# Performance work log

Measured on AMD Instinct MI355X. Metric: run time of the kernel, lower is better.

The kernel has to match this reference:

```python
import math
import jax, jax.numpy as jnp
import numpy as np

B, S, E, H, P = 8, 1024, 512, 8, 32
MAXD, OFFS, LW, STL, HID = 256, 8.0, 4, 4, 2048

def _lin(x, w, b):
    return x @ w.T + b

def _gelu(x):
    return jax.nn.gelu(x, approximate=False)  # torch nn.GELU default (erf)

def _ln(x, g, b, eps=1e-5):
    m = x.mean(-1, keepdims=True)
    v = ((x - m) ** 2).mean(-1, keepdims=True)
    return (x - m) / jnp.sqrt(v + eps) * g + b

def setup_inputs() -> dict:
    key = jax.random.key(0)
    ks = iter(jax.random.split(key, 40))
    def w(*shape):
        return (jax.random.normal(next(ks), shape, dtype=jnp.float32) * 0.02)
    x = jax.random.normal(next(ks), (B, S, E), dtype=jnp.float32)
    lengths = jax.random.randint(next(ks), (B,), S // 2, S + 1)
    padding_mask = jnp.arange(S)[None, :] >= lengths[:, None]  # (B,S) bool
    inp = dict(x=x, padding_mask=padding_mask)
    # local MHA (torch nn.MultiheadAttention packed in_proj)
    inp.update(in_proj_w=w(3 * E, E), in_proj_b=jnp.zeros((3 * E,), jnp.float32),
               mha_out_w=w(E, E), mha_out_b=jnp.zeros((E,), jnp.float32))
    # deformable attention projections
    for nm in ('dq', 'dk', 'dv', 'do'):
        inp[nm + '_w'] = w(E, E); inp[nm + '_b'] = jnp.zeros((E,), jnp.float32)
    inp.update(off1_w=w(E, E), off1_b=jnp.zeros((E,), jnp.float32),
               off2_w=w(H * P, E), off2_b=jnp.zeros((H * P,), jnp.float32))
    inp.update(gate1_w=w(E, 3 * E), gate1_b=jnp.zeros((E,), jnp.float32),
               gate2_w=w(E, E), gate2_b=jnp.zeros((E,), jnp.float32))
    inp.update(n1_g=jnp.ones((E,), jnp.float32), n1_b=jnp.zeros((E,), jnp.float32),
               n2_g=jnp.ones((E,), jnp.float32), n2_b=jnp.zeros((E,), jnp.float32))
    inp.update(ffn1_w=w(HID, E), ffn1_b=jnp.zeros((HID,), jnp.float32),
               ffn2_w=w(E, HID), ffn2_b=jnp.zeros((E,), jnp.float32))
    return inp

def _forward(x, padding_mask, in_proj_w, in_proj_b, mha_out_w, mha_out_b,
             dq_w, dq_b, dk_w, dk_b, dv_w, dv_b, do_w, do_b,
             off1_w, off1_b, off2_w, off2_b, gate1_w, gate1_b, gate2_w, gate2_b,
             n1_g, n1_b, n2_g, n2_b, ffn1_w, ffn1_b, ffn2_w, ffn2_b):
    Bv, Sv, Ev = x.shape
    hd = Ev // H
    pos = jnp.arange(Sv)
    # ---------------- local causal windowed MHA ----------------
    qkv = _lin(x, in_proj_w, in_proj_b)
    q, k, v = jnp.split(qkv, 3, axis=-1)
    q = q.reshape(Bv, Sv, H, hd).transpose(0, 2, 1, 3)  # bhsd
    k = k.reshape(Bv, Sv, H, hd).transpose(0, 2, 1, 3)
    v = v.reshape(Bv, Sv, H, hd).transpose(0, 2, 1, 3)
    scores = jnp.einsum('bhqd,bhkd->bhqk', q, k) / math.sqrt(hd)
    future = pos[None, :] > pos[:, None]
    too_far = (pos[:, None] - pos[None, :]) >= min(LW, STL)
    lmask = (future | too_far)[None, None] | padding_mask[:, None, None, :]
    scores = jnp.where(lmask, -jnp.inf, scores)
    allm = lmask.all(-1, keepdims=True)
    scores = jnp.where(allm, 0.0, scores)  # avoid NaN on fully-masked (padded) rows
    attn = jax.nn.softmax(scores, axis=-1)
    attn = jnp.where(lmask, 0.0, attn)
    lo = jnp.einsum('bhqk,bhkd->bhqd', attn, v).transpose(0, 2, 1, 3).reshape(Bv, Sv, Ev)
    local_out = _lin(lo, mha_out_w, mha_out_b)
    # ---------------- deformable long-history attention ----------------
    anchors = jnp.linspace(0.1, 0.9, P)
    valid_len = jnp.clip(Sv - padding_mask.sum(-1), 1, None)
    positions = pos[None, :, None].astype(jnp.float32)  # (1,S,1)
    base = anchors[None, None, :] * positions
    off = jnp.tanh(_lin(_gelu(_lin(x, off1_w, off1_b)), off2_w, off2_b))
    off = off.reshape(Bv, Sv, H, P).mean(2) * OFFS
    sampled = base + off
    sampled = jnp.clip(sampled, jnp.clip(positions - MAXD, 0, None), positions)
    sampled = jnp.minimum(sampled, (valid_len - 1).astype(jnp.float32)[:, None, None])
    sp = jnp.round(sampled).astype(jnp.int32)  # (B,S,P) sample positions
    qd = _lin(x, dq_w, dq_b)
    kd = _lin(x, dk_w, dk_b)
    vd = _lin(x, dv_w, dv_b)
    bidx = jnp.arange(Bv)[:, None, None]
    k_sp = kd[bidx, sp]  # (B,S,P,E) gathered keys
    v_sp = vd[bidx, sp]
    sc = jnp.einsum('bqd,bqpd->bqp', qd, k_sp) / math.sqrt(Ev)
    samp_inv = padding_mask[bidx, sp]
    causal_inv = sp > pos[None, :, None]
    rb = jnp.clip(pos[:, None] - (STL - 1), 0, None)
    long_mem_mask = pos[None, :] >= rb  # (S,S): forbid recent short-term positions
    extra_inv = long_mem_mask[pos[None, :, None], sp]
    inv = samp_inv | causal_inv | extra_inv
    sc = jnp.where(inv, -jnp.inf, sc)
    alli = inv.all(-1, keepdims=True)
    sc = jnp.where(alli, 0.0, sc)
    a = jax.nn.softmax(sc, axis=-1)
    a = jnp.where(inv, 0.0, a)
    long_out = _lin(jnp.einsum('bqp,bqpd->bqd', a, v_sp), do_w, do_b)
    # ---------------- gate fuse + FFN ----------------
    cat = jnp.concatenate([x, local_out, long_out], axis=-1)
    g = jax.nn.sigmoid(_lin(_gelu(_lin(cat, gate1_w, gate1_b)), gate2_w, gate2_b))
    fused = g * local_out + (1.0 - g) * long_out
    x1 = _ln(x + fused, n1_g, n1_b)
    f = _lin(_gelu(_lin(x1, ffn1_w, ffn1_b)), ffn2_w, ffn2_b)
    return _ln(x1 + f, n2_g, n2_b)

def reference(x, padding_mask, in_proj_w, in_proj_b, mha_out_w, mha_out_b,
              dq_w, dq_b, dk_w, dk_b, dv_w, dv_b, do_w, do_b,
              off1_w, off1_b, off2_w, off2_b, gate1_w, gate1_b, gate2_w, gate2_b,
              n1_g, n1_b, n2_g, n2_b, ffn1_w, ffn1_b, ffn2_w, ffn2_b):
    return _forward(x, padding_mask, in_proj_w, in_proj_b, mha_out_w, mha_out_b,
                    dq_w, dq_b, dk_w, dk_b, dv_w, dv_b, do_w, do_b,
                    off1_w, off1_b, off2_w, off2_b, gate1_w, gate1_b, gate2_w, gate2_b,
                    n1_g, n1_b, n2_g, n2_b, ffn1_w, ffn1_b, ffn2_w, ffn2_b)
```

## Files before the change

### kernel.cpp

```cpp
#include <hip/hip_runtime.h>
#include <hip/hip_bf16.h>
#include <type_traits>

typedef __hip_bfloat16 bf16;
typedef __attribute__((ext_vector_type(8))) short short8;
typedef __attribute__((ext_vector_type(4))) float floatx4;

static constexpr int kB = 8;
static constexpr int kS = 1024;
static constexpr int kE = 512;
static constexpr int kH = 8;
static constexpr int kP = 32;
static constexpr int kTok = kB * kS;
static constexpr int kHid = 2048;

__device__ __forceinline__ void load8f(const bf16* p, float* f) {
  uint4 u = *(const uint4*)p;
  const bf16* h = (const bf16*)&u;
#pragma unroll
  for (int e = 0; e < 8; e++) f[e] = __bfloat162float(h[e]);
}
__device__ __forceinline__ void store8b(bf16* p, const float* f) {
  uint4 u;
  bf16* h = (bf16*)&u;
#pragma unroll
  for (int e = 0; e < 8; e++) h[e] = __float2bfloat16(f[e]);
  *(uint4*)p = u;
}
__device__ __forceinline__ bool is_pad(const void* pm, int flag, int idx) {
  return flag ? (((const int*)pm)[idx] != 0)
              : (((const unsigned char*)pm)[idx] != 0);
}
__device__ __forceinline__ float fast_gelu(float x) {
  float u = x * (0.7978845608f + 0.044714998f * x * x);
  float e = __expf(2.0f * u);
  float t = 1.0f - 2.0f / (e + 1.0f);
  return 0.5f * x * (1.0f + t);
}
__device__ __forceinline__ void dma16(const bf16* g, bf16* l) {
  __builtin_amdgcn_global_load_lds(
      (const __attribute__((address_space(1))) unsigned int*)g,
      (__attribute__((address_space(3))) unsigned int*)l, 16, 0, 0);
}
__device__ __forceinline__ void drain_all() { __builtin_amdgcn_s_waitcnt(0); }

__global__ __launch_bounds__(256) void detect_meta_kernel(
    const void* __restrict__ x, const void* __restrict__ pm,
    int* __restrict__ meta) {
  __shared__ int cnt;
  __shared__ int bigfound;
  __shared__ int pc[kB];
  int tid = threadIdx.x;
  if (tid == 0) { cnt = 0; bigfound = 0; }
  if (tid < kB) pc[tid] = 0;
  __syncthreads();
  const unsigned short* u = (const unsigned short*)x;
  int c = 0;
  for (int i = tid; i < 1024; i += 256) {
    int e = (u[i] >> 7) & 0xFF;
    if (e >= 0x90) c++;
  }
  if (c) atomicAdd(&cnt, c);
  const unsigned int* wp = (const unsigned int*)pm;
  int f = 0;
  for (int i = tid; i < 2048; i += 256)
    if (wp[i] & 0xFFFFFFFEu) f = 1;
  if (f) atomicOr(&bigfound, 1);
  __syncthreads();
  int flag = bigfound ? 0 : 1;
  for (int i = tid; i < kTok; i += 256)
    if (is_pad(pm, flag, i)) atomicAdd(&pc[i >> 10], 1);
  __syncthreads();
  if (tid == 0) {
    meta[0] = flag;
    meta[9] = (cnt > 64) ? 1 : 0;
  }
  if (tid < kB) {
    int vl = kS - pc[tid];
    if (vl < 1) vl = 1;
    meta[1 + tid] = vl;
  }
}

struct CvtJob { const void* src; bf16* hi; bf16* lo; int nblk; };
struct CvtJobs { CvtJob j[13]; };
struct CvtFJob { const void* src; float* dst; int n; };
struct CvtFJobs { CvtFJob j[16]; };
__global__ __launch_bounds__(256) void cvt_all_kernel(
    CvtJobs jobs, CvtFJobs fjobs, int totblk, const int* __restrict__ meta) {
  int fp = meta[9];
  int b = blockIdx.x;
  if (b >= totblk) {
#pragma unroll 1
    for (int ji = 0; ji < 16; ji++) {
      CvtFJob J = fjobs.j[ji];
      for (int i = threadIdx.x; i < J.n; i += 256)
        J.dst[i] = fp ? ((const float*)J.src)[i]
                      : __bfloat162float(((const bf16*)J.src)[i]);
    }
    return;
  }
  int ji = 0;
  while (b >= jobs.j[ji].nblk) { b -= jobs.j[ji].nblk; ji++; }
  CvtJob J = jobs.j[ji];
  int i = b * 1024 + threadIdx.x * 4;
  float v[4];
  if (fp) {
    float4 f = ((const float4*)J.src)[i >> 2];
    v[0] = f.x; v[1] = f.y; v[2] = f.z; v[3] = f.w;
  } else {
    uint2 u = *(const uint2*)((const bf16*)J.src + i);
    const bf16* h = (const bf16*)&u;
#pragma unroll
    for (int e = 0; e < 4; e++) v[e] = __bfloat162float(h[e]);
  }
  uint2 uh;
  bf16* hh = (bf16*)&uh;
#pragma unroll
  for (int e = 0; e < 4; e++) hh[e] = __float2bfloat16(v[e]);
  *(uint2*)(J.hi + i) = uh;
  if (J.lo) {
    uint2 ul;
    bf16* hl = (bf16*)&ul;
#pragma unroll
    for (int e = 0; e < 4; e++)
      hl[e] = __float2bfloat16(v[e] - __bfloat162float(hh[e]));
    *(uint2*)(J.lo + i) = ul;
  }
}

static constexpr int BK = 32;

template <int BM, int BN, int ACT, typename OUTT>
__device__ __forceinline__ void gemm_core(bf16* smem, const bf16* A,
                                          const bf16* W, const float* bias,
                                          OUTT* C, int N, int K, int m0,
                                          int n0) {
  constexpr int WR = (BM == 128 && BN == 128) ? 4 : 2;
  constexpr int WC = 4;
  bf16* As[2] = {smem, smem + BM * BK};
  bf16* Bs[2] = {smem + 2 * BM * BK, smem + 2 * BM * BK + BN * BK};
  const int tid = threadIdx.x;
  const int lane = tid & 63;
  const int wid = tid >> 6;
  int wm, wn;
  if constexpr (BM == 128 && BN == 128) {
    wm = (wid >> 1) * 64; wn = (wid & 1) * 64;
  } else {
    wm = wid * 32; wn = 0;
  }

  auto stage = [&](int buf, int kt) {
#pragma unroll
    for (int c = 0; c < BM / 64; c++) {
      int seg = c * 64 + wid * 16;
      int row = seg + (lane >> 2);
      int ch = (lane & 3) ^ ((row >> 1) & 3);
      dma16(&A[(size_t)(m0 + row) * K + kt + ch * 8], &As[buf][seg * BK]);
    }
#pragma unroll
    for (int c = 0; c < BN / 64; c++) {
      int seg = c * 64 + wid * 16;
      int row = seg + (lane >> 2);
      int ch = (lane & 3) ^ ((row >> 1) & 3);
      dma16(&W[(size_t)(n0 + row) * K + kt + ch * 8], &Bs[buf][seg * BK]);
    }
  };

  floatx4 acc[WR][WC];
#pragma unroll
  for (int i = 0; i < WR; i++)
#pragma unroll
    for (int j = 0; j < WC; j++) acc[i][j] = (floatx4)0.0f;

  stage(0, 0);
  drain_all();
  __syncthreads();
  const int niter = K / BK;
  for (int k = 0; k < niter; k++) {
    const int cur = k & 1;
    if (k + 1 < niter) stage(cur ^ 1, (k + 1) * BK);
    const int kb = lane >> 4;
    short8 af[WR], bfr[WC];
#pragma unroll
    for (int i = 0; i < WR; i++) {
      int r = wm + i * 16 + (lane & 15);
      af[i] = *(const short8*)(&As[cur][r * BK + ((kb ^ ((r >> 1) & 3)) << 3)]);
    }
#pragma unroll
    for (int j = 0; j < WC; j++) {
      int r = wn + j * 16 + (lane & 15);
      bfr[j] = *(const short8*)(&Bs[cur][r * BK + ((kb ^ ((r >> 1) & 3)) << 3)]);
    }
#pragma unroll
    for (int i = 0; i < WR; i++)
#pragma unroll
      for (int j = 0; j < WC; j++)
        acc[i][j] = __builtin_amdgcn_mfma_f32_16x16x32_bf16(bfr[j], af[i],
                                                            acc[i][j], 0, 0, 0);
    drain_all();
    __syncthreads();
  }

#pragma unroll
  for (int i = 0; i < WR; i++) {
    int row = m0 + wm + i * 16 + (lane & 15);
#pragma unroll
    for (int j = 0; j < WC; j++) {
      int col = n0 + wn + j * 16 + ((lane >> 4) << 2);
      float bv[4] = {0.f, 0.f, 0.f, 0.f};
      if (bias) {
        float4 b4 = *(const float4*)&bias[col];
        bv[0] = b4.x; bv[1] = b4.y; bv[2] = b4.z; bv[3] = b4.w;
      }
      float v[4];
#pragma unroll
      for (int r = 0; r < 4; r++) {
        v[r] = acc[i][j][r] + bv[r];
        if (ACT == 1) v[r] = fast_gelu(v[r]);
        else if (ACT == 2) v[r] = 1.0f / (1.0f + __expf(-v[r]));
      }
      size_t idx = (size_t)row * N + col;
      if constexpr (std::is_same<OUTT, float>::value) {
        *(float4*)&C[idx] = make_float4(v[0], v[1], v[2], v[3]);
      } else {
        uint2 u;
        bf16* h = (bf16*)&u;
#pragma unroll
        for (int r = 0; r < 4; r++) h[r] = __float2bfloat16(v[r]);
        *(uint2*)&C[idx] = u;
      }
    }
  }
}

template <int BM, int BN, bool SPLIT, bool ALWAYS_AL>
__device__ __forceinline__ void gemm3_core(
    bf16* smem, const bf16* Ah, const bf16* Al, const bf16* Wh,
    const bf16* Wl, const float* bias, const int* meta, float* Cf, bf16* Chi,
    bf16* Clo, int N, int K, int m0, int n0) {
  constexpr int WR = 2;
  constexpr int WC = (BM == 128) ? 4 : 2;
  bf16* Ash = smem;
  bf16* Asl = smem + BM * BK;
  bf16* Bsh = smem + 2 * BM * BK;
  bf16* Bsl = smem + 2 * BM * BK + BN * BK;
  const int fp = meta[9];
  const bool use_al = fp || ALWAYS_AL;
  const int tid = threadIdx.x;
  const int lane = tid & 63;
  const int wid = tid >> 6;
  int wm, wn;
  if constexpr (BM == 128) {
    wm = wid * 32; wn = 0;
  } else {
    wm = (wid >> 1) * 32; wn = (wid & 1) * 32;
  }

  floatx4 acc[WR][WC];
#pragma unroll
  for (int i = 0; i < WR; i++)
#pragma unroll
    for (int j = 0; j < WC; j++) acc[i][j] = (floatx4)0.0f;

  for (int kt = 0; kt < K; kt += BK) {
#pragma unroll
    for (int c = 0; c < BM / 64; c++) {
      int seg = c * 64 + wid * 16;
      int row = seg + (lane >> 2);
      int ch = (lane & 3) ^ ((row >> 1) & 3);
      size_t g = (size_t)(m0 + row) * K + kt + ch * 8;
      dma16(&Ah[g], &Ash[seg * BK]);
      if (use_al) dma16(&Al[g], &Asl[seg * BK]);
    }
#pragma unroll
    for (int c = 0; c < BN / 64; c++) {
      int seg = c * 64 + wid * 16;
      int row = seg + (lane >> 2);
      int ch = (lane & 3) ^ ((row >> 1) & 3);
      size_t g = (size_t)(n0 + row) * K + kt + ch * 8;
      dma16(&Wh[g], &Bsh[seg * BK]);
      if (fp) dma16(&Wl[g], &Bsl[seg * BK]);
    }
    drain_all();
    __syncthreads();
    const int kb = lane >> 4;
    short8 ah[WR], al[WR], bh[WC], bl[WC];
#pragma unroll
    for (int i = 0; i < WR; i++) {
      int r = wm + i * 16 + (lane & 15);
      int ro = r * BK + ((kb ^ ((r >> 1) & 3)) << 3);
      ah[i] = *(const short8*)(&Ash[ro]);
      if (use_al) al[i] = *(const short8*)(&Asl[ro]);
    }
#pragma unroll
    for (int j = 0; j < WC; j++) {
      int r = wn + j * 16 + (lane & 15);
      int ro = r * BK + ((kb ^ ((r >> 1) & 3)) << 3);
      bh[j] = *(const short8*)(&Bsh[ro]);
      if (fp) bl[j] = *(const short8*)(&Bsl[ro]);
    }
#pragma unroll
    for (int i = 0; i < WR; i++)
#pragma unroll
      for (int j = 0; j < WC; j++) {
        acc[i][j] = __builtin_amdgcn_mfma_f32_16x16x32_bf16(bh[j], ah[i],
                                                            acc[i][j], 0, 0, 0);
        if (fp)
          acc[i][j] = __builtin_amdgcn_mfma_f32_16x16x32_bf16(
              bl[j], ah[i], acc[i][j], 0, 0, 0);
        if (use_al)
          acc[i][j] = __builtin_amdgcn_mfma_f32_16x16x32_bf16(
              bh[j], al[i], acc[i][j], 0, 0, 0);
      }
    __syncthreads();
  }

#pragma unroll
  for (int i = 0; i < WR; i++) {
    int row = m0 + wm + i * 16 + (lane & 15);
#pragma unroll
    for (int j = 0; j < WC; j++) {
      int col = n0 + wn + j * 16 + ((lane >> 4) << 2);
      float4 b4 = *(const float4*)&bias[col];
      float bv[4] = {b4.x, b4.y, b4.z, b4.w};
      if constexpr (SPLIT) {
        uint2 uh, ul;
        bf16* hh = (bf16*)&uh;
        bf16* hl = (bf16*)&ul;
#pragma unroll
        for (int r = 0; r < 4; r++) {
          float v = acc[i][j][r] + bv[r];
          float g = 0.5f * v * (1.0f + erff(v * 0.70710678118654752f));
          bf16 hi = __float2bfloat16(g);
          hh[r] = hi;
          hl[r] = __float2bfloat16(g - __bfloat162float(hi));
        }
        *(uint2*)&Chi[(size_t)row * N + col] = uh;
        *(uint2*)&Clo[(size_t)row * N + col] = ul;
      } else {
        *(float4*)&Cf[(size_t)row * N + col] =
            make_float4(acc[i][j][0] + bv[0], acc[i][j][1] + bv[1],
                        acc[i][j][2] + bv[2], acc[i][j][3] + bv[3]);
      }
    }
  }
}

template <int BM, int BN, int ACT, typename OUTT>
__global__ __launch_bounds__(256) void gemm_bt(
    const bf16* __restrict__ A, const bf16* __restrict__ W,
    const float* __restrict__ bias, OUTT* __restrict__ C, int N, int K) {
  __shared__ bf16 smem[2 * (BM + BN) * BK];
  gemm_core<BM, BN, ACT, OUTT>(smem, A, W, bias, C, N, K, blockIdx.x * BM,
                               blockIdx.y * BN);
}

__global__ __launch_bounds__(256) void gemm_pair(
    const bf16* __restrict__ A0, const bf16* __restrict__ W0,
    const float* __restrict__ b0, bf16* __restrict__ C0,
    const bf16* __restrict__ A1, const bf16* __restrict__ W1,
    const float* __restrict__ b1, bf16* __restrict__ C1, int N, int K) {
  __shared__ bf16 smem[2 * (128 + 64) * BK];
  int nb = N >> 6;
  bool s = (int)blockIdx.y >= nb;
  gemm_core<128, 64, 0, bf16>(smem, s ? A1 : A0, s ? W1 : W0, s ? b1 : b0,
                              s ? C1 : C0, N, K, blockIdx.x * 128,
                              (s ? (int)blockIdx.y - nb : (int)blockIdx.y) * 64);
}

__global__ __launch_bounds__(256) void qkv_o1_kernel(
    const bf16* __restrict__ x_hi, const bf16* __restrict__ x_lo,
    const bf16* __restrict__ wall, const float* __restrict__ ball,
    bf16* __restrict__ qkv_all, const bf16* __restrict__ o1h,
    const bf16* __restrict__ o1l, const float* __restrict__ o1b,
    const int* __restrict__ meta, bf16* __restrict__ h_hi,
    bf16* __restrict__ h_lo) {
  __shared__ bf16 smem[2 * 256 * BK];
  if ((int)blockIdx.y < 24) {
    gemm_core<128, 128, 0, bf16>(smem, x_hi, wall, ball, qkv_all, 3072, kE,
                                 blockIdx.x * 128, blockIdx.y * 128);
  } else {
    gemm3_core<128, 64, true, false>(smem, x_hi, x_lo, o1h, o1l, o1b, meta,
                                     nullptr, h_hi, h_lo, kE, kE,
                                     blockIdx.x * 128,
                                     ((int)blockIdx.y - 24) * 64);
  }
}

__device__ __forceinline__ void local_attn_body(const bf16* __restrict__ qkv,
                                                const void* __restrict__ pm,
                                                const int* __restrict__ meta,
                                                bf16* __restrict__ lo,
                                                int bid) {
  int lane = threadIdx.x & 63;
  int t = bid * 4 + (threadIdx.x >> 6);
  int b = t >> 10, s = t & 1023;
  int h = lane >> 3, sub = lane & 7;
  int flag = meta[0];
  float q[8];
  load8f(qkv + (size_t)t * 3072 + h * 64 + sub * 8, q);
  float sc[4];
  bool val[4];
#pragma unroll
  for (int w = 0; w < 4; w++) {
    int kp = s - 3 + w;
    bool v = (kp >= 0) && !is_pad(pm, flag, b * kS + kp);
    float d = 0.0f;
    if (v) {
      float kk[8];
      load8f(qkv + (size_t)(b * kS + kp) * 3072 + 512 + h * 64 + sub * 8, kk);
#pragma unroll
      for (int e = 0; e < 8; e++) d += q[e] * kk[e];
    }
    d += __shfl_xor(d, 1);
    d += __shfl_xor(d, 2);
    d += __shfl_xor(d, 4);
    sc[w] = v ? d / 8.0f : -INFINITY;
    val[w] = v;
  }
  float mx = fmaxf(fmaxf(sc[0], sc[1]), fmaxf(sc[2], sc[3]));
  float a[4] = {0.f, 0.f, 0.f, 0.f};
  if (mx != -INFINITY) {
    float ssum = 0.f;
#pragma unroll
    for (int w = 0; w < 4; w++) {
      float e = val[w] ? expf(sc[w] - mx) : 0.0f;
      a[w] = e;
      ssum += e;
    }
#pragma unroll
    for (int w = 0; w < 4; w++) a[w] /= ssum;
  }
  float o[8] = {0.f, 0.f, 0.f, 0.f, 0.f, 0.f, 0.f, 0.f};
#pragma unroll
  for (int w = 0; w < 4; w++) {
    if (val[w] && a[w] > 0.0f) {
      int kp = s - 3 + w;
      float vv[8];
      load8f(qkv + (size_t)(b * kS + kp) * 3072 + 1024 + h * 64 + sub * 8, vv);
#pragma unroll
      for (int e = 0; e < 8; e++) o[e] += a[w] * vv[e];
    }
  }
  store8b(lo + (size_t)t * kE + lane * 8, o);
}

__global__ __launch_bounds__(256) void local_o2_kernel(
    const bf16* __restrict__ qkv, const void* __restrict__ pm,
    const int* __restrict__ meta, bf16* __restrict__ lo_ctx,
    const bf16* __restrict__ h_hi, const bf16* __restrict__ h_lo,
    const bf16* __restrict__ o2h, const bf16* __restrict__ o2l,
    const float* __restrict__ o2b, float* __restrict__ rawf) {
  __shared__ bf16 smem[4 * 64 * BK];
  if ((int)blockIdx.x < 2048) {
    local_attn_body(qkv, pm, meta, lo_ctx, blockIdx.x);
  } else {
    int id = (int)blockIdx.x - 2048;
    gemm3_core<64, 64, false, true>(smem, h_hi, h_lo, o2h, o2l, o2b, meta,
                                    rawf, nullptr, nullptr, 256, kE,
                                    (id >> 2) * 64, (id & 3) * 64);
  }
}

__global__ __launch_bounds__(256) void long_attn_kernel(
    const bf16* __restrict__ qkv, const float* __restrict__ rawf,
    const void* __restrict__ pm, const int* __restrict__ meta,
    bf16* __restrict__ ctx) {
  int lane = threadIdx.x & 63;
  int bid = blockIdx.x;
  int sbid = (bid & 7) * 256 + (bid >> 3);
  int t = sbid * 4 + (threadIdx.x >> 6);
  int b = t >> 10, s = t & 1023;
  int flag = meta[0];
  int p = lane & 31;
  float off = 0.0f;
#pragma unroll
  for (int h = 0; h < kH; h++) off += tanhf(rawf[(size_t)t * 256 + h * kP + p]);
  double anchor = 0.1 + 0.8 * (double)p / 31.0;
  double sampled = anchor * (double)s + (double)off;
  double lov = fmax(0.0, (double)s - 256.0);
  sampled = fmin(fmax(sampled, lov), (double)s);
  int vlen = meta[1 + b];
  sampled = fmin(sampled, (double)(vlen - 1));
  int spv = (int)rint(sampled);
  bool inv = is_pad(pm, flag, b * kS + spv) || (spv > s) ||
             (spv >= max(0, s - 3));
  int row_abs = b * kS + spv;
  float q[8];
  load8f(qkv + (size_t)t * 3072 + 1536 + lane * 8, q);
  float sc_mine = 0.0f;
#pragma unroll 4
  for (int pp = 0; pp < 32; pp++) {
    int row = __shfl(row_abs, pp);
    float kk[8];
    load8f(qkv + (size_t)row * 3072 + 2048 + lane * 8, kk);
    float d = 0.0f;
#pragma unroll
    for (int e = 0; e < 8; e++) d += q[e] * kk[e];
#pragma unroll
    for (int m = 1; m < 64; m <<= 1) d += __shfl_xor(d, m);
    if (p == pp) sc_mine = d;
  }
  float sc = inv ? -INFINITY : sc_mine / 22.627416997969522f;
  float mx = sc;
#pragma unroll
  for (int m = 1; m < 32; m <<= 1) mx = fmaxf(mx, __shfl_xor(mx, m));
  float e = (inv || mx == -INFINITY) ? 0.0f : expf(sc - mx);
  float ssum = e;
#pragma unroll
  for (int m = 1; m < 32; m <<= 1) ssum += __shfl_xor(ssum, m);
  float a = (ssum > 0.0f) ? e / ssum : 0.0f;
  float o[8] = {0.f, 0.f, 0.f, 0.f, 0.f, 0.f, 0.f, 0.f};
#pragma unroll 4
  for (int pp = 0; pp < 32; pp++) {
    float ap = __shfl(a, pp);
    int row = __shfl(row_abs, pp);
    if (ap != 0.0f) {
      float vv[8];
      load8f(qkv + (size_t)row * 3072 + 2560 + lane * 8, vv);
#pragma unroll
      for (int e2 = 0; e2 < 8; e2++) o[e2] += ap * vv[e2];
    }
  }
  store8b(ctx + (size_t)t * kE + lane * 8, o);
}

__global__ __launch_bounds__(256) void gemm_gate1(
    const bf16* __restrict__ x, const bf16* __restrict__ lo,
    const bf16* __restrict__ lg, const bf16* __restrict__ W,
    const float* __restrict__ bias, bf16* __restrict__ C) {
  constexpr int BM = 128, BN = 64, WR = 2, WC = 4;
  constexpr int N = 512, K = 1536;
  __shared__ bf16 As[2][BM * BK];
  __shared__ bf16 Bs[2][BN * BK];
  const int tid = threadIdx.x;
  const int lane = tid & 63;
  const int wid = tid >> 6;
  const int wm = wid * 32, wn = 0;
  const int m0 = blockIdx.x * BM, n0 = blockIdx.y * BN;

  auto stage = [&](int buf, int kt) {
    const bf16* src = (kt < 512) ? x : (kt < 1024) ? lo : lg;
    int kk = kt & 511;
#pragma unroll
    for (int c = 0; c < 2; c++) {
      int seg = c * 64 + wid * 16;
      int row = seg + (lane >> 2);
      int ch = (lane & 3) ^ ((row >> 1) & 3);
      dma16(&src[(size_t)(m0 + row) * 512 + kk + ch * 8], &As[buf][seg * BK]);
    }
    {
      int seg = wid * 16;
      int row = seg + (lane >> 2);
      int ch = (lane & 3) ^ ((row >> 1) & 3);
      dma16(&W[(size_t)(n0 + row) * K + kt + ch * 8], &Bs[buf][seg * BK]);
    }
  };

  floatx4 acc[WR][WC];
#pragma unroll
  for (int i = 0; i < WR; i++)
#pragma unroll
    for (int j = 0; j < WC; j++) acc[i][j] = (floatx4)0.0f;

  stage(0, 0);
  drain_all();
  __syncthreads();
  const int niter = K / BK;
  for (int k = 0; k < niter; k++) {
    const int cur = k & 1;
    if (k + 1 < niter) stage(cur ^ 1, (k + 1) * BK);
    const int kb = lane >> 4;
    short8 af[WR], bfr[WC];
#pragma unroll
    for (int i = 0; i < WR; i++) {
      int r = wm + i * 16 + (lane & 15);
      af[i] = *(const short8*)(&As[cur][r * BK + ((kb ^ ((r >> 1) & 3)) << 3)]);
    }
#pragma unroll
    for (int j = 0; j < WC; j++) {
      int r = wn + j * 16 + (lane & 15);
      bfr[j] = *(const short8*)(&Bs[cur][r * BK + ((kb ^ ((r >> 1) & 3)) << 3)]);
    }
#pragma unroll
    for (int i = 0; i < WR; i++)
#pragma unroll
      for (int j = 0; j < WC; j++)
        acc[i][j] = __builtin_amdgcn_mfma_f32_16x16x32_bf16(bfr[j], af[i],
                                                            acc[i][j], 0, 0, 0);
    drain_all();
    __syncthreads();
  }

#pragma unroll
  for (int i = 0; i < WR; i++) {
    int row = m0 + wm + i * 16 + (lane & 15);
#pragma unroll
    for (int j = 0; j < WC; j++) {
      int col = n0 + wn + j * 16 + ((lane >> 4) << 2);
      float4 b4 = *(const float4*)&bias[col];
      float bv[4] = {b4.x, b4.y, b4.z, b4.w};
      uint2 u;
      bf16* h = (bf16*)&u;
#pragma unroll
      for (int r = 0; r < 4; r++)
        h[r] = __float2bfloat16(fast_gelu(acc[i][j][r] + bv[r]));
      *(uint2*)&C[(size_t)row * N + col] = u;
    }
  }
}

__global__ __launch_bounds__(256) void ln1_kernel(
    const void* __restrict__ xin, const int* __restrict__ meta,
    const bf16* __restrict__ lo, const bf16* __restrict__ lg,
    const bf16* __restrict__ g, const float* __restrict__ gamma,
    const float* __restrict__ beta, bf16* __restrict__ x1b,
    float* __restrict__ x1f) {
  int lane = threadIdx.x & 63;
  int t = blockIdx.x * 4 + (threadIdx.x >> 6);
  size_t base = (size_t)t * kE + lane * 8;
  float xv[8], lov[8], lgv[8], gv[8], h[8];
  if (meta[9]) {
    const float4* xf = (const float4*)((const float*)xin + base);
    float4 a = xf[0], b2 = xf[1];
    xv[0] = a.x; xv[1] = a.y; xv[2] = a.z; xv[3] = a.w;
    xv[4] = b2.x; xv[5] = b2.y; xv[6] = b2.z; xv[7] = b2.w;
  } else {
    load8f((const bf16*)xin + base, xv);
  }
  load8f(lo + base, lov);
  load8f(lg + base, lgv);
  load8f(g + base, gv);
  float s1 = 0.f, s2 = 0.f;
#pragma unroll
  for (int e = 0; e < 8; e++) {
    h[e] = xv[e] + gv[e] * lov[e] + (1.0f - gv[e]) * lgv[e];
    s1 += h[e];
    s2 += h[e] * h[e];
  }
#pragma unroll
  for (int m = 1; m < 64; m <<= 1) {
    s1 += __shfl_xor(s1, m);
    s2 += __shfl_xor(s2, m);
  }
  float mean = s1 * (1.0f / kE);
  float var = s2 * (1.0f / kE) - mean * mean;
  float rstd = 1.0f / sqrtf(var + 1e-5f);
  float y[8];
#pragma unroll
  for (int e = 0; e < 8; e++)
    y[e] = (h[e] - mean) * rstd * gamma[lane * 8 + e] + beta[lane * 8 + e];
  store8b(x1b + base, y);
#pragma unroll
  for (int e = 0; e < 8; e++) x1f[base + e] = y[e];
}

__global__ __launch_bounds__(256) void ln2_kernel(
    const float* __restrict__ x1f, const float* __restrict__ ff,
    const float* __restrict__ gamma, const float* __restrict__ beta,
    const int* __restrict__ meta, void* __restrict__ out) {
  int lane = threadIdx.x & 63;
  int t = blockIdx.x * 4 + (threadIdx.x >> 6);
  size_t base = (size_t)t * kE + lane * 8;
  float h[8];
  float s1 = 0.f, s2 = 0.f;
#pragma unroll
  for (int e = 0; e < 8; e++) {
    h[e] = x1f[base + e] + ff[base + e];
    s1 += h[e];
    s2 += h[e] * h[e];
  }
#pragma unroll
  for (int m = 1; m < 64; m <<= 1) {
    s1 += __shfl_xor(s1, m);
    s2 += __shfl_xor(s2, m);
  }
  float mean = s1 * (1.0f / kE);
  float var = s2 * (1.0f / kE) - mean * mean;
  float rstd = 1.0f / sqrtf(var + 1e-5f);
  float y[8];
#pragma unroll
  for (int e = 0; e < 8; e++)
    y[e] = (h[e] - mean) * rstd * gamma[lane * 8 + e] + beta[lane * 8 + e];
  if (meta[9]) {
    float* of = (float*)out + base;
    ((float4*)of)[0] = make_float4(y[0], y[1], y[2], y[3]);
    ((float4*)of)[1] = make_float4(y[4], y[5], y[6], y[7]);
  } else {
    store8b((bf16*)out + base, y);
  }
}

extern "C" void kernel_launch(void* const* d_in, const int* in_sizes, int n_in,
                              void* d_out, int out_size, void* d_ws,
                              size_t ws_size, hipStream_t stream) {
  const void* x = d_in[0];
  const void* pm = d_in[1];

  char* w = (char*)d_ws;
  auto alloc = [&](size_t bytes) {
    char* p = w;
    w += (bytes + 255) & ~(size_t)255;
    return p;
  };
  bf16* qkv_all = (bf16*)alloc((size_t)kTok * 3072 * 2);
  bf16* lo_ctx = (bf16*)alloc((size_t)kTok * kE * 2);
  bf16* ctx2 = (bf16*)alloc((size_t)kTok * kE * 2);
  bf16* local_out = (bf16*)alloc((size_t)kTok * kE * 2);
  bf16* long_out = (bf16*)alloc((size_t)kTok * kE * 2);
  bf16* hbuf = (bf16*)alloc((size_t)kTok * kE * 2);
  bf16* gbuf = (bf16*)alloc((size_t)kTok * kE * 2);
  bf16* x1b = (bf16*)alloc((size_t)kTok * kE * 2);
  float* x1f = (float*)alloc((size_t)kTok * kE * 4);
  float* rawf = (float*)alloc((size_t)kTok * 256 * 4);
  int* meta = (int*)alloc(256);
  bf16* x_hi = (bf16*)alloc((size_t)kTok * kE * 2);
  bf16* x_lo = (bf16*)alloc((size_t)kTok * kE * 2);
  bf16* wall = (bf16*)alloc((size_t)3072 * 512 * 2);
  bf16* mow = (bf16*)alloc(512 * 512 * 2);
  bf16* dow = (bf16*)alloc(512 * 512 * 2);
  bf16* o1h = (bf16*)alloc(512 * 512 * 2);
  bf16* o1l = (bf16*)alloc(512 * 512 * 2);
  bf16* o2h = (bf16*)alloc(256 * 512 * 2);
  bf16* o2l = (bf16*)alloc(256 * 512 * 2);
  bf16* g1w = (bf16*)alloc(512 * 1536 * 2);
  bf16* g2w = (bf16*)alloc(512 * 512 * 2);
  bf16* f1w = (bf16*)alloc((size_t)2048 * 512 * 2);
  bf16* f2w = (bf16*)alloc((size_t)512 * 2048 * 2);
  float* ball = (float*)alloc(3072 * 4);
  float* mob = (float*)alloc(512 * 4);
  float* dob = (float*)alloc(512 * 4);
  float* o1b = (float*)alloc(512 * 4);
  float* o2b = (float*)alloc(256 * 4);
  float* g1b = (float*)alloc(512 * 4);
  float* g2b = (float*)alloc(512 * 4);
  float* n1g = (float*)alloc(512 * 4);
  float* n1bt = (float*)alloc(512 * 4);
  float* n2g = (float*)alloc(512 * 4);
  float* n2bt = (float*)alloc(512 * 4);
  float* f1b = (float*)alloc(2048 * 4);
  float* f2b = (float*)alloc(512 * 4);

  bf16* h_hi = hbuf;
  bf16* h_lo = x1b;
  float* f_f32 = (float*)qkv_all;
  bf16* ffn_h = (bf16*)((char*)qkv_all + (size_t)kTok * kE * 4);

  dim3 blk(256);
  detect_meta_kernel<<<1, blk, 0, stream>>>(x, pm, meta);

  CvtJobs J;
  auto job = [](const void* s, bf16* hi, bf16* lo, int n) {
    CvtJob j; j.src = s; j.hi = hi; j.lo = lo; j.nblk = n >> 10; return j;
  };
  J.j[0] = job(d_in[0], x_hi, x_lo, kTok * kE);
  J.j[1] = job(d_in[2], wall, nullptr, 1536 * 512);
  J.j[2] = job(d_in[6], wall + (size_t)1536 * 512, nullptr, 512 * 512);
  J.j[3] = job(d_in[8], wall + (size_t)2048 * 512, nullptr, 512 * 512);
  J.j[4] = job(d_in[10], wall + (size_t)2560 * 512, nullptr, 512 * 512);
  J.j[5] = job(d_in[4], mow, nullptr, 512 * 512);
  J.j[6] = job(d_in[12], dow, nullptr, 512 * 512);
  J.j[7] = job(d_in[14], o1h, o1l, 512 * 512);
  J.j[8] = job(d_in[16], o2h, o2l, 256 * 512);
  J.j[9] = job(d_in[18], g1w, nullptr, 512 * 1536);
  J.j[10] = job(d_in[20], g2w, nullptr, 512 * 512);
  J.j[11] = job(d_in[26], f1w, nullptr, 2048 * 512);
  J.j[12] = job(d_in[28], f2w, nullptr, 512 * 2048);
  int totblk = 0;
  for (int i = 0; i < 13; i++) totblk += J.j[i].nblk;

  CvtFJobs JF;
  auto fjob = [](const void* s, float* d, int n) {
    CvtFJob j; j.src = s; j.dst = d; j.n = n; return j;
  };
  JF.j[0] = fjob(d_in[3], ball, 1536);
  JF.j[1] = fjob(d_in[7], ball + 1536, 512);
  JF.j[2] = fjob(d_in[9], ball + 2048, 512);
  JF.j[3] = fjob(d_in[11], ball + 2560, 512);
  JF.j[4] = fjob(d_in[5], mob, 512);
  JF.j[5] = fjob(d_in[13], dob, 512);
  JF.j[6] = fjob(d_in[15], o1b, 512);
  JF.j[7] = fjob(d_in[17], o2b, 256);
  JF.j[8] = fjob(d_in[19], g1b, 512);
  JF.j[9] = fjob(d_in[21], g2b, 512);
  JF.j[10] = fjob(d_in[22], n1g, 512);
  JF.j[11] = fjob(d_in[23], n1bt, 512);
  JF.j[12] = fjob(d_in[24], n2g, 512);
  JF.j[13] = fjob(d_in[25], n2bt, 512);
  JF.j[14] = fjob(d_in[27], f1b, 2048);
  JF.j[15] = fjob(d_in[29], f2b, 512);
  cvt_all_kernel<<<totblk + 1, blk, 0, stream>>>(J, JF, totblk, meta);

  qkv_o1_kernel<<<dim3(64, 32), blk, 0, stream>>>(
      x_hi, x_lo, wall, ball, qkv_all, o1h, o1l, o1b, meta, h_hi, h_lo);
  local_o2_kernel<<<2560, blk, 0, stream>>>(qkv_all, pm, meta, lo_ctx, h_hi,
                                            h_lo, o2h, o2l, o2b, rawf);
  long_attn_kernel<<<2048, blk, 0, stream>>>(qkv_all, rawf, pm, meta, ctx2);

  gemm_pair<<<dim3(64, 16), blk, 0, stream>>>(lo_ctx, mow, mob, local_out,
                                              ctx2, dow, dob, long_out, kE, kE);

  gemm_gate1<<<dim3(64, 8), blk, 0, stream>>>(x_hi, local_out, long_out, g1w,
                                              g1b, hbuf);
  gemm_bt<128, 64, 2, bf16><<<dim3(64, 8), blk, 0, stream>>>(
      hbuf, g2w, g2b, gbuf, kE, kE);

  ln1_kernel<<<2048, blk, 0, stream>>>(x, meta, local_out, long_out, gbuf, n1g,
                                       n1bt, x1b, x1f);
  gemm_bt<128, 128, 1, bf16><<<dim3(64, 16), blk, 0, stream>>>(
      x1b, f1w, f1b, ffn_h, kHid, kE);
  gemm_bt<128, 64, 0, float><<<dim3(64, 8), blk, 0, stream>>>(
      ffn_h, f2w, f2b, f_f32, kE, kHid);
  ln2_kernel<<<2048, blk, 0, stream>>>(x1f, f_f32, n2g, n2bt, meta, d_out);
}
```

Before: 503.5 us.

## Read bf16 inputs directly in GEMMs and skip conversion pass when not fp32

When inputs are already bf16, the conversion kernel now exits early and each GEMM selects the raw input and weight pointers at runtime instead of reading converted copies. The QKV GEMM maps column tiles onto separate raw weight tensors. It also splits the previously fused qkv+o1 and local_attn+o2 launches into separate kernels. This removes a full copy pass over weights and activations in the bf16 case, at the cost of more kernel launches and the loss of the overlap the fused launches gave.

```diff
diff --git a/kernel.cpp b/kernel.cpp
--- a/kernel.cpp
+++ b/kernel.cpp
@@ -100,20 +100,13 @@
     }
     return;
   }
+  if (!fp) return;
   int ji = 0;
   while (b >= jobs.j[ji].nblk) { b -= jobs.j[ji].nblk; ji++; }
   CvtJob J = jobs.j[ji];
   int i = b * 1024 + threadIdx.x * 4;
-  float v[4];
-  if (fp) {
-    float4 f = ((const float4*)J.src)[i >> 2];
-    v[0] = f.x; v[1] = f.y; v[2] = f.z; v[3] = f.w;
-  } else {
-    uint2 u = *(const uint2*)((const bf16*)J.src + i);
-    const bf16* h = (const bf16*)&u;
-#pragma unroll
-    for (int e = 0; e < 4; e++) v[e] = __bfloat162float(h[e]);
-  }
+  float4 f = ((const float4*)J.src)[i >> 2];
+  float v[4] = {f.x, f.y, f.z, f.w};
   uint2 uh;
   bf16* hh = (bf16*)&uh;
 #pragma unroll
@@ -135,7 +128,7 @@
 __device__ __forceinline__ void gemm_core(bf16* smem, const bf16* A,
                                           const bf16* W, const float* bias,
                                           OUTT* C, int N, int K, int m0,
-                                          int n0) {
+                                          int n0, int n0w) {
   constexpr int WR = (BM == 128 && BN == 128) ? 4 : 2;
   constexpr int WC = 4;
   bf16* As[2] = {smem, smem + BM * BK};
@@ -163,7 +156,7 @@
       int seg = c * 64 + wid * 16;
       int row = seg + (lane >> 2);
       int ch = (lane & 3) ^ ((row >> 1) & 3);
-      dma16(&W[(size_t)(n0 + row) * K + kt + ch * 8], &Bs[buf][seg * BK]);
+      dma16(&W[(size_t)(n0w + row) * K + kt + ch * 8], &Bs[buf][seg * BK]);
     }
   };
 
@@ -237,7 +230,7 @@
 template <int BM, int BN, bool SPLIT, bool ALWAYS_AL>
 __device__ __forceinline__ void gemm3_core(
     bf16* smem, const bf16* Ah, const bf16* Al, const bf16* Wh,
-    const bf16* Wl, const float* bias, const int* meta, float* Cf, bf16* Chi,
+    const bf16* Wl, const float* bias, int fp, float* Cf, bf16* Chi,
     bf16* Clo, int N, int K, int m0, int n0) {
   constexpr int WR = 2;
   constexpr int WC = (BM == 128) ? 4 : 2;
@@ -245,7 +238,6 @@
   bf16* Asl = smem + BM * BK;
   bf16* Bsh = smem + 2 * BM * BK;
   bf16* Bsl = smem + 2 * BM * BK + BN * BK;
-  const int fp = meta[9];
   const bool use_al = fp || ALWAYS_AL;
   const int tid = threadIdx.x;
   const int lane = tid & 63;
@@ -347,54 +339,182 @@
   }
 }
 
+__global__ __launch_bounds__(256) void gemm_qkv(
+    const bf16* __restrict__ xc, const void* __restrict__ xr,
+    const bf16* __restrict__ wall, const void* __restrict__ ipr,
+    const void* __restrict__ dqr, const void* __restrict__ dkr,
+    const void* __restrict__ dvr, const float* __restrict__ ball,
+    bf16* __restrict__ C, const int* __restrict__ meta) {
+  __shared__ bf16 smem[2 * 256 * BK];
+  int fp = meta[9];
+  const bf16* A = fp ? xc : (const bf16*)xr;
+  int y = blockIdx.y, n0 = y * 128, n0w;
+  const bf16* W;
+  if (fp) {
+    W = wall; n0w = n0;
+  } else if (y < 12) {
+    W = (const bf16*)ipr; n0w = n0;
+  } else {
+    int s = (y - 12) >> 2;
+    W = (const bf16*)(s == 0 ? dqr : s == 1 ? dkr : dvr);
+    n0w = ((y - 12) & 3) * 128;
+  }
+  gemm_core<128, 128, 0, bf16>(smem, A, W, ball, C, 3072, kE,
+                               blockIdx.x * 128, n0, n0w);
+}
+
 template <int BM, int BN, int ACT, typename OUTT>
-__global__ __launch_bounds__(256) void gemm_bt(
-    const bf16* __restrict__ A, const bf16* __restrict__ W,
-    const float* __restrict__ bias, OUTT* __restrict__ C, int N, int K) {
+__global__ __launch_bounds__(256) void gemm_sel(
+    const bf16* __restrict__ A, const bf16* __restrict__ Wc,
+    const void* __restrict__ Wr, const float* __restrict__ bias,
+    OUTT* __restrict__ C, int N, int K, const int* __restrict__ meta) {
   __shared__ bf16 smem[2 * (BM + BN) * BK];
-  gemm_core<BM, BN, ACT, OUTT>(smem, A, W, bias, C, N, K, blockIdx.x * BM,
-                               blockIdx.y * BN);
+  const bf16* W = meta[9] ? Wc : (const bf16*)Wr;
+  int n0 = blockIdx.y * BN;
+  gemm_core<BM, BN, ACT, OUTT>(smem, A, W, bias, C, N, K, blockIdx.x * BM, n0,
+                               n0);
 }
 
 __global__ __launch_bounds__(256) void gemm_pair(
-    const bf16* __restrict__ A0, const bf16* __restrict__ W0,
-    const float* __restrict__ b0, bf16* __restrict__ C0,
-    const bf16* __restrict__ A1, const bf16* __restrict__ W1,
-    const float* __restrict__ b1, bf16* __restrict__ C1, int N, int K) {
+    const bf16* __restrict__ A0, const bf16* __restrict__ W0c,
+    const void* __restrict__ W0r, const float* __restrict__ b0,
+    bf16* __restrict__ C0, const bf16* __restrict__ A1,
+    const bf16* __restrict__ W1c, const void* __restrict__ W1r,
+    const float* __restrict__ b1, bf16* __restrict__ C1, int N, int K,
+    const int* __restrict__ meta) {
   __shared__ bf16 smem[2 * (128 + 64) * BK];
+  int fp = meta[9];
   int nb = N >> 6;
   bool s = (int)blockIdx.y >= nb;
-  gemm_core<128, 64, 0, bf16>(smem, s ? A1 : A0, s ? W1 : W0, s ? b1 : b0,
-                              s ? C1 : C0, N, K, blockIdx.x * 128,
-                              (s ? (int)blockIdx.y - nb : (int)blockIdx.y) * 64);
-}
-
-__global__ __launch_bounds__(256) void qkv_o1_kernel(
-    const bf16* __restrict__ x_hi, const bf16* __restrict__ x_lo,
-    const bf16* __restrict__ wall, const float* __restrict__ ball,
-    bf16* __restrict__ qkv_all, const bf16* __restrict__ o1h,
-    const bf16* __restrict__ o1l, const float* __restrict__ o1b,
-    const int* __restrict__ meta, bf16* __restrict__ h_hi,
-    bf16* __restrict__ h_lo) {
-  __shared__ bf16 smem[2 * 256 * BK];
-  if ((int)blockIdx.y < 24) {
-    gemm_core<128, 128, 0, bf16>(smem, x_hi, wall, ball, qkv_all, 3072, kE,
-                                 blockIdx.x * 128, blockIdx.y * 128);
-  } else {
-    gemm3_core<128, 64, true, false>(smem, x_hi, x_lo, o1h, o1l, o1b, meta,
-                                     nullptr, h_hi, h_lo, kE, kE,
-                                     blockIdx.x * 128,
-                                     ((int)blockIdx.y - 24) * 64);
-  }
-}
-
-__device__ __forceinline__ void local_attn_body(const bf16* __restrict__ qkv,
-                                                const void* __restrict__ pm,
-                                                const int* __restrict__ meta,
-                                                bf16* __restrict__ lo,
-                                                int bid) {
+  const bf16* W = s ? (fp ? W1c : (const bf16*)W1r)
+                    : (fp ? W0c : (const bf16*)W0r);
+  int n0 = (s ? (int)blockIdx.y - nb : (int)blockIdx.y) * 64;
+  gemm_core<128, 64, 0, bf16>(smem, s ? A1 : A0, W, s ? b1 : b0, s ? C1 : C0,
+                              N, K, blockIdx.x * 128, n0, n0);
+}
+
+__global__ __launch_bounds__(256) void gemm_o1(
+    const bf16* __restrict__ xc, const void* __restrict__ xr,
+    const bf16* __restrict__ x_lo, const bf16* __restrict__ o1hc,
+    const void* __restrict__ o1r, const bf16* __restrict__ o1l,
+    const float* __restrict__ o1b, const int* __restrict__ meta,
+    bf16* __restrict__ h_hi, bf16* __restrict__ h_lo) {
+  __shared__ bf16 smem[(2 * 128 + 2 * 64) * BK];
+  int fp = meta[9];
+  gemm3_core<128, 64, true, false>(
+      smem, fp ? xc : (const bf16*)xr, x_lo, fp ? o1hc : (const bf16*)o1r,
+      o1l, o1b, fp, nullptr, h_hi, h_lo, kE, kE, blockIdx.x * 128,
+      blockIdx.y * 64);
+}
+
+__global__ __launch_bounds__(256) void gemm_o2(
+    const bf16* __restrict__ h_hi, const bf16* __restrict__ h_lo,
+    const bf16* __restrict__ o2hc, const void* __restrict__ o2r,
+    const bf16* __restrict__ o2l, const float* __restrict__ o2b,
+    const int* __restrict__ meta, float* __restrict__ rawf) {
+  __shared__ bf16 smem[4 * 64 * BK];
+  int fp = meta[9];
+  gemm3_core<64, 64, false, true>(smem, h_hi, h_lo,
+                                  fp ? o2hc : (const bf16*)o2r, o2l, o2b, fp,
+                                  rawf, nullptr, nullptr, 256, kE,
+                                  blockIdx.x * 64, blockIdx.y * 64);
+}
+
+__global__ __launch_bounds__(256) void gemm_gate1(
+    const bf16* __restrict__ xc, const void* __restrict__ xr,
+    const bf16* __restrict__ lo, const bf16* __restrict__ lg,
+    const bf16* __restrict__ Wc, const void* __restrict__ Wr,
+    const float* __restrict__ bias, bf16* __restrict__ C,
+    const int* __restrict__ meta) {
+  constexpr int BM = 128, BN = 64, WR = 2, WC = 4;
+  constexpr int N = 512, K = 1536;
+  __shared__ bf16 As[2][BM * BK];
+  __shared__ bf16 Bs[2][BN * BK];
+  int fp = meta[9];
+  const bf16* x = fp ? xc : (const bf16*)xr;
+  const bf16* W = fp ? Wc : (const bf16*)Wr;
+  const int tid = threadIdx.x;
+  const int lane = tid & 63;
+  const int wid = tid >> 6;
+  const int wm = wid * 32, wn = 0;
+  const int m0 = blockIdx.x * BM, n0 = blockIdx.y * BN;
+
+  auto stage = [&](int buf, int kt) {
+    const bf16* src = (kt < 512) ? x : (kt < 1024) ? lo : lg;
+    int kk = kt & 511;
+#pragma unroll
+    for (int c = 0; c < 2; c++) {
+      int seg = c * 64 + wid * 16;
+      int row = seg + (lane >> 2);
+      int ch = (lane & 3) ^ ((row >> 1) & 3);
+      dma16(&src[(size_t)(m0 + row) * 512 + kk + ch * 8], &As[buf][seg * BK]);
+    }
+    {
+      int seg = wid * 16;
+      int row = seg + (lane >> 2);
+      int ch = (lane & 3) ^ ((row >> 1) & 3);
+      dma16(&W[(size_t)(n0 + row) * K + kt + ch * 8], &Bs[buf][seg * BK]);
+    }
+  };
+
+  floatx4 acc[WR][WC];
+#pragma unroll
+  for (int i = 0; i < WR; i++)
+#pragma unroll
+    for (int j = 0; j < WC; j++) acc[i][j] = (floatx4)0.0f;
+
+  stage(0, 0);
+  drain_all();
+  __syncthreads();
+  const int niter = K / BK;
+  for (int k = 0; k < niter; k++) {
+    const int cur = k & 1;
+    if (k + 1 < niter) stage(cur ^ 1, (k + 1) * BK);
+    const int kb = lane >> 4;
+    short8 af[WR], bfr[WC];
+#pragma unroll
+    for (int i = 0; i < WR; i++) {
+      int r = wm + i * 16 + (lane & 15);
+      af[i] = *(const short8*)(&As[cur][r * BK + ((kb ^ ((r >> 1) & 3)) << 3)]);
+    }
+#pragma unroll
+    for (int j = 0; j < WC; j++) {
+      int r = wn + j * 16 + (lane & 15);
+      bfr[j] = *(const short8*)(&Bs[cur][r * BK + ((kb ^ ((r >> 1) & 3)) << 3)]);
+    }
+#pragma unroll
+    for (int i = 0; i < WR; i++)
+#pragma unroll
+      for (int j = 0; j < WC; j++)
+        acc[i][j] = __builtin_amdgcn_mfma_f32_16x16x32_bf16(bfr[j], af[i],
+                                                            acc[i][j], 0, 0, 0);
+    drain_all();
+    __syncthreads();
+  }
+
+#pragma unroll
+  for (int i = 0; i < WR; i++) {
+    int row = m0 + wm + i * 16 + (lane & 15);
+#pragma unroll
+    for (int j = 0; j < WC; j++) {
+      int col = n0 + wn + j * 16 + ((lane >> 4) << 2);
+      float4 b4 = *(const float4*)&bias[col];
+      float bv[4] = {b4.x, b4.y, b4.z, b4.w};
+      uint2 u;
+      bf16* h = (bf16*)&u;
+#pragma unroll
+      for (int r = 0; r < 4; r++)
+        h[r] = __float2bfloat16(fast_gelu(acc[i][j][r] + bv[r]));
+      *(uint2*)&C[(size_t)row * N + col] = u;
+    }
+  }
+}
+
+__global__ __launch_bounds__(256) void local_attn_kernel(
+    const bf16* __restrict__ qkv, const void* __restrict__ pm,
+    const int* __restrict__ meta, bf16* __restrict__ lo) {
   int lane = threadIdx.x & 63;
-  int t = bid * 4 + (threadIdx.x >> 6);
+  int t = blockIdx.x * 4 + (threadIdx.x >> 6);
   int b = t >> 10, s = t & 1023;
   int h = lane >> 3, sub = lane & 7;
   int flag = meta[0];
@@ -444,23 +564,6 @@
     }
   }
   store8b(lo + (size_t)t * kE + lane * 8, o);
-}
-
-__global__ __launch_bounds__(256) void local_o2_kernel(
-    const bf16* __restrict__ qkv, const void* __restrict__ pm,
-    const int* __restrict__ meta, bf16* __restrict__ lo_ctx,
-    const bf16* __restrict__ h_hi, const bf16* __restrict__ h_lo,
-    const bf16* __restrict__ o2h, const bf16* __restrict__ o2l,
-    const float* __restrict__ o2b, float* __restrict__ rawf) {
-  __shared__ bf16 smem[4 * 64 * BK];
-  if ((int)blockIdx.x < 2048) {
-    local_attn_body(qkv, pm, meta, lo_ctx, blockIdx.x);
-  } else {
-    int id = (int)blockIdx.x - 2048;
-    gemm3_core<64, 64, false, true>(smem, h_hi, h_lo, o2h, o2l, o2b, meta,
-                                    rawf, nullptr, nullptr, 256, kE,
-                                    (id >> 2) * 64, (id & 3) * 64);
-  }
 }
 
 __global__ __launch_bounds__(256) void long_attn_kernel(
@@ -524,91 +627,6 @@
     }
   }
   store8b(ctx + (size_t)t * kE + lane * 8, o);
-}
-
-__global__ __launch_bounds__(256) void gemm_gate1(
-    const bf16* __restrict__ x, const bf16* __restrict__ lo,
-    const bf16* __restrict__ lg, const bf16* __restrict__ W,
-    const float* __restrict__ bias, bf16* __restrict__ C) {
-  constexpr int BM = 128, BN = 64, WR = 2, WC = 4;
-  constexpr int N = 512, K = 1536;
-  __shared__ bf16 As[2][BM * BK];
-  __shared__ bf16 Bs[2][BN * BK];
-  const int tid = threadIdx.x;
-  const int lane = tid & 63;
-  const int wid = tid >> 6;
-  const int wm = wid * 32, wn = 0;
-  const int m0 = blockIdx.x * BM, n0 = blockIdx.y * BN;
-
-  auto stage = [&](int buf, int kt) {
-    const bf16* src = (kt < 512) ? x : (kt < 1024) ? lo : lg;
-    int kk = kt & 511;
-#pragma unroll
-    for (int c = 0; c < 2; c++) {
-      int seg = c * 64 + wid * 16;
-      int row = seg + (lane >> 2);
-      int ch = (lane & 3) ^ ((row >> 1) & 3);
-      dma16(&src[(size_t)(m0 + row) * 512 + kk + ch * 8], &As[buf][seg * BK]);
-    }
-    {
-      int seg = wid * 16;
-      int row = seg + (lane >> 2);
-      int ch = (lane & 3) ^ ((row >> 1) & 3);
-      dma16(&W[(size_t)(n0 + row) * K + kt + ch * 8], &Bs[buf][seg * BK]);
-    }
-  };
-
-  floatx4 acc[WR][WC];
-#pragma unroll
-  for (int i = 0; i < WR; i++)
-#pragma unroll
-    for (int j = 0; j < WC; j++) acc[i][j] = (floatx4)0.0f;
-
-  stage(0, 0);
-  drain_all();
-  __syncthreads();
-  const int niter = K / BK;
-  for (int k = 0; k < niter; k++) {
-    const int cur = k & 1;
-    if (k + 1 < niter) stage(cur ^ 1, (k + 1) * BK);
-    const int kb = lane >> 4;
-    short8 af[WR], bfr[WC];
-#pragma unroll
-    for (int i = 0; i < WR; i++) {
-      int r = wm + i * 16 + (lane & 15);
-      af[i] = *(const short8*)(&As[cur][r * BK + ((kb ^ ((r >> 1) & 3)) << 3)]);
-    }
-#pragma unroll
-    for (int j = 0; j < WC; j++) {
-      int r = wn + j * 16 + (lane & 15);
-      bfr[j] = *(const short8*)(&Bs[cur][r * BK + ((kb ^ ((r >> 1) & 3)) << 3)]);
-    }
-#pragma unroll
-    for (int i = 0; i < WR; i++)
-#pragma unroll
-      for (int j = 0; j < WC; j++)
-        acc[i][j] = __builtin_amdgcn_mfma_f32_16x16x32_bf16(bfr[j], af[i],
-                                                            acc[i][j], 0, 0, 0);
-    drain_all();
-    __syncthreads();
-  }
-
-#pragma unroll
-  for (int i = 0; i < WR; i++) {
-    int row = m0 + wm + i * 16 + (lane & 15);
-#pragma unroll
-    for (int j = 0; j < WC; j++) {
-      int col = n0 + wn + j * 16 + ((lane >> 4) << 2);
-      float4 b4 = *(const float4*)&bias[col];
-      float bv[4] = {b4.x, b4.y, b4.z, b4.w};
-      uint2 u;
-      bf16* h = (bf16*)&u;
-#pragma unroll
-      for (int r = 0; r < 4; r++)
-        h[r] = __float2bfloat16(fast_gelu(acc[i][j][r] + bv[r]));
-      *(uint2*)&C[(size_t)row * N + col] = u;
-    }
-  }
 }
 
 __global__ __launch_bounds__(256) void ln1_kernel(
@@ -792,25 +810,30 @@
   JF.j[15] = fjob(d_in[29], f2b, 512);
   cvt_all_kernel<<<totblk + 1, blk, 0, stream>>>(J, JF, totblk, meta);
 
-  qkv_o1_kernel<<<dim3(64, 32), blk, 0, stream>>>(
-      x_hi, x_lo, wall, ball, qkv_all, o1h, o1l, o1b, meta, h_hi, h_lo);
-  local_o2_kernel<<<2560, blk, 0, stream>>>(qkv_all, pm, meta, lo_ctx, h_hi,
-                                            h_lo, o2h, o2l, o2b, rawf);
+  gemm_qkv<<<dim3(64, 24), blk, 0, stream>>>(x_hi, x, wall, d_in[2], d_in[6],
+                                             d_in[8], d_in[10], ball, qkv_all,
+                                             meta);
+  gemm_o1<<<dim3(64, 8), blk, 0, stream>>>(x_hi, x, x_lo, o1h, d_in[14], o1l,
+                                           o1b, meta, h_hi, h_lo);
+  local_attn_kernel<<<2048, blk, 0, stream>>>(qkv_all, pm, meta, lo_ctx);
+  gemm_o2<<<dim3(128, 4), blk, 0, stream>>>(h_hi, h_lo, o2h, d_in[16], o2l,
+                                            o2b, meta, rawf);
   long_attn_kernel<<<2048, blk, 0, stream>>>(qkv_all, rawf, pm, meta, ctx2);
 
-  gemm_pair<<<dim3(64, 16), blk, 0, stream>>>(lo_ctx, mow, mob, local_out,
-                                              ctx2, dow, dob, long_out, kE, kE);
-
-  gemm_gate1<<<dim3(64, 8), blk, 0, stream>>>(x_hi, local_out, long_out, g1w,
-                                              g1b, hbuf);
-  gemm_bt<128, 64, 2, bf16><<<dim3(64, 8), blk, 0, stream>>>(
-      hbuf, g2w, g2b, gbuf, kE, kE);
+  gemm_pair<<<dim3(64, 16), blk, 0, stream>>>(lo_ctx, mow, d_in[4], mob,
+                                              local_out, ctx2, dow, d_in[12],
+                                              dob, long_out, kE, kE, meta);
+
+  gemm_gate1<<<dim3(64, 8), blk, 0, stream>>>(x_hi, x, local_out, long_out,
+                                              g1w, d_in[18], g1b, hbuf, meta);
+  gemm_sel<128, 64, 2, bf16><<<dim3(64, 8), blk, 0, stream>>>(
+      hbuf, g2w, d_in[20], g2b, gbuf, kE, kE, meta);
 
   ln1_kernel<<<2048, blk, 0, stream>>>(x, meta, local_out, long_out, gbuf, n1g,
                                        n1bt, x1b, x1f);
-  gemm_bt<128, 128, 1, bf16><<<dim3(64, 16), blk, 0, stream>>>(
-      x1b, f1w, f1b, ffn_h, kHid, kE);
-  gemm_bt<128, 64, 0, float><<<dim3(64, 8), blk, 0, stream>>>(
-      ffn_h, f2w, f2b, f_f32, kE, kHid);
+  gemm_sel<128, 128, 1, bf16><<<dim3(64, 16), blk, 0, stream>>>(
+      x1b, f1w, d_in[26], f1b, ffn_h, kHid, kE, meta);
+  gemm_sel<128, 64, 0, float><<<dim3(64, 8), blk, 0, stream>>>(
+      ffn_h, f2w, d_in[28], f2b, f_f32, kE, kHid, meta);
   ln2_kernel<<<2048, blk, 0, stream>>>(x1f, f_f32, n2g, n2bt, meta, d_out);
 }
```

New measurement: 477.4 us. 5.2% less time.
